# Kernel tuning notes

Hardware: AMD Instinct MI355X
Metric: run time of the kernel (lower is better)

## Reference

```python
import jax, jax.numpy as jnp
import numpy as np

NUM_CLASSES = 80
FOCAL_ALPHA = 0.25
FOCAL_GAMMA = 2.0
HUBER_SIGMA = 3.0
REG_MEAN = 0.0
REG_STD = 0.2
IMG_H = 800.0
IMG_W = 800.0
B, A, M = 4, 100000, 32


def setup_inputs() -> dict:
    key = jax.random.key(0)
    k1, k2, k3, k4, k5, k6, k7 = jax.random.split(key, 7)
    classification = jax.random.uniform(k1, (B, A, NUM_CLASSES), dtype=jnp.float32)
    regression = jax.random.normal(k2, (B, A, 4), dtype=jnp.float32)
    # plausible anchors: centers inside image, sizes 16..256
    cx = jax.random.uniform(k3, (A,), minval=0.0, maxval=IMG_W)
    cy = jax.random.uniform(k4, (A,), minval=0.0, maxval=IMG_H)
    s = jax.random.uniform(k5, (A, 2), minval=16.0, maxval=256.0)
    anchors = jnp.stack([cx - s[:, 0] / 2, cy - s[:, 1] / 2,
                         cx + s[:, 0] / 2, cy + s[:, 1] / 2], axis=1).astype(jnp.float32)
    # annotations: [B, M, 5] = x1,y1,x2,y2,class
    xy = jax.random.uniform(k6, (B, M, 2), minval=0.0, maxval=650.0)
    wh = jax.random.uniform(k7, (B, M, 2), minval=30.0, maxval=150.0)
    cls = jax.random.randint(jax.random.fold_in(key, 9), (B, M, 1), 0, NUM_CLASSES).astype(jnp.float32)
    annotations = jnp.concatenate([xy, xy + wh, cls], axis=-1)
    return {"classification": classification, "regression": regression,
            "anchors": anchors, "annotations": annotations}


def _pairwise_iou(anchors, boxes):
    # anchors [A,4], boxes [M,4] -> [A,M]
    ix1 = jnp.maximum(anchors[:, None, 0], boxes[None, :, 0])
    iy1 = jnp.maximum(anchors[:, None, 1], boxes[None, :, 1])
    ix2 = jnp.minimum(anchors[:, None, 2], boxes[None, :, 2])
    iy2 = jnp.minimum(anchors[:, None, 3], boxes[None, :, 3])
    inter = jnp.clip(ix2 - ix1, 0.0) * jnp.clip(iy2 - iy1, 0.0)
    area_a = (anchors[:, 2] - anchors[:, 0]) * (anchors[:, 3] - anchors[:, 1])
    area_b = (boxes[:, 2] - boxes[:, 0]) * (boxes[:, 3] - boxes[:, 1])
    union = area_a[:, None] + area_b[None, :] - inter
    return inter / jnp.maximum(union, 1e-8)


def _targets(anchors, annotations):
    # per-image anchor assignment, vmapped over batch
    def per_image(ann):
        boxes = ann[:, :4]
        cls = ann[:, 4].astype(jnp.int32)
        ious = _pairwise_iou(anchors, boxes)          # [A,M]
        best = jnp.argmax(ious, axis=1)               # [A]
        best_iou = jnp.max(ious, axis=1)
        pos = best_iou >= 0.5
        ign = (best_iou > 0.4) & (~pos)
        states = jnp.where(pos, 1.0, jnp.where(ign, -1.0, 0.0))
        cx = (anchors[:, 0] + anchors[:, 2]) * 0.5
        cy = (anchors[:, 1] + anchors[:, 3]) * 0.5
        inside = (cx >= 0) & (cx < IMG_W) & (cy >= 0) & (cy < IMG_H)
        states = jnp.where(inside, states, -1.0)
        labels = jax.nn.one_hot(cls[best], NUM_CLASSES, dtype=jnp.float32) * pos[:, None]
        ab = boxes[best]                              # assigned gt boxes [A,4]
        aw = anchors[:, 2] - anchors[:, 0]
        ah = anchors[:, 3] - anchors[:, 1]
        t = jnp.stack([(ab[:, 0] - anchors[:, 0]) / aw,
                       (ab[:, 1] - anchors[:, 1]) / ah,
                       (ab[:, 2] - anchors[:, 2]) / aw,
                       (ab[:, 3] - anchors[:, 3]) / ah], axis=1)
        t = (t - REG_MEAN) / REG_STD
        return labels, t, states
    return jax.vmap(per_image)(annotations)


def reference(classification, regression, anchors, annotations):
    labels, reg_t, states = _targets(anchors, annotations)   # [B,A,K],[B,A,4],[B,A]
    num_pos = jnp.maximum(jnp.sum((states == 1.0).astype(jnp.float32)), 1.0)
    # focal loss over non-ignored anchors
    valid = (states != -1.0)[..., None].astype(jnp.float32)
    p = jnp.clip(classification, 1e-4, 1.0 - 1e-4)
    bce = -(labels * jnp.log(p) + (1.0 - labels) * jnp.log1p(-p))
    alpha_f = jnp.where(labels == 1.0, FOCAL_ALPHA, 1.0 - FOCAL_ALPHA)
    focal_w = alpha_f * jnp.where(labels == 1.0, 1.0 - p, p) ** FOCAL_GAMMA
    cls_loss = jnp.sum(focal_w * bce * valid) / num_pos
    # smooth L1 over positive anchors
    pos_m = (states == 1.0)[..., None].astype(jnp.float32)
    s2 = HUBER_SIGMA ** 2
    d = jnp.abs(regression - reg_t)
    l1 = jnp.where(d < 1.0 / s2, 0.5 * s2 * d * d, d - 0.5 / s2)
    reg_loss = jnp.sum(l1 * pos_m) / num_pos
    return cls_loss + reg_loss
```

## Files before the change

kernel.cpp:

```cpp
#include <hip/hip_runtime.h>

#define BB 4
#define AA 100000
#define MM 32
#define NC 80
#define GX 391
#define NBLK (GX * BB)


__global__ __launch_bounds__(256) void fused_kernel(
    const float* __restrict__ anchors,
    const float* __restrict__ annotations,
    const float* __restrict__ regression,
    const float* __restrict__ cls,
    float* __restrict__ cls_part,
    float* __restrict__ reg_part,
    unsigned* __restrict__ pos_part)
{
    __shared__ float ann[MM * 5];
    __shared__ int scode[256];
    const int b = blockIdx.y;
    const int tid = threadIdx.x;
    if (tid < MM * 5) ann[tid] = annotations[b * MM * 5 + tid];
    __syncthreads();

    const int abase = blockIdx.x * 256;
    const int a = abase + tid;
    float reg_sum = 0.0f;
    int pos_cnt = 0;
    int code = -2;

    if (a < AA) {
        const float4 an = ((const float4*)anchors)[a];
        const float ax1 = an.x, ay1 = an.y, ax2 = an.z, ay2 = an.w;
        const float area_a = __fmul_rn(__fsub_rn(ax2, ax1), __fsub_rn(ay2, ay1));

        float best_iou = -1.0f;
        int best = 0;
        #pragma unroll
        for (int j = 0; j < MM; ++j) {
            const float bx1 = ann[j * 5 + 0];
            const float by1 = ann[j * 5 + 1];
            const float bx2 = ann[j * 5 + 2];
            const float by2 = ann[j * 5 + 3];
            const float ix1 = fmaxf(ax1, bx1);
            const float iy1 = fmaxf(ay1, by1);
            const float ix2 = fminf(ax2, bx2);
            const float iy2 = fminf(ay2, by2);
            const float iw = fmaxf(__fsub_rn(ix2, ix1), 0.0f);
            const float ih = fmaxf(__fsub_rn(iy2, iy1), 0.0f);
            const float inter = __fmul_rn(iw, ih);
            const float area_b = __fmul_rn(__fsub_rn(bx2, bx1), __fsub_rn(by2, by1));
            const float uni = __fsub_rn(__fadd_rn(area_a, area_b), inter);
            const float iou = __fdiv_rn(inter, fmaxf(uni, 1e-8f));
            if (iou > best_iou) { best_iou = iou; best = j; }
        }

        const bool pos = best_iou >= 0.5f;
        const bool ign = (best_iou > 0.4f) && !pos;
        const float cx = (ax1 + ax2) * 0.5f;
        const float cy = (ay1 + ay2) * 0.5f;
        const bool inside = (cx >= 0.0f) && (cx < 800.0f) && (cy >= 0.0f) && (cy < 800.0f);

        const bool valid = inside && !ign;
        if (valid) code = pos ? (int)ann[best * 5 + 4] : -1;

        if (pos && inside) {
            pos_cnt = 1;
            const float aw = ax2 - ax1;
            const float ah = ay2 - ay1;
            const float bx1 = ann[best * 5 + 0];
            const float by1 = ann[best * 5 + 1];
            const float bx2 = ann[best * 5 + 2];
            const float by2 = ann[best * 5 + 3];
            float t[4];
            t[0] = ((bx1 - ax1) / aw) / 0.2f;
            t[1] = ((by1 - ay1) / ah) / 0.2f;
            t[2] = ((bx2 - ax2) / aw) / 0.2f;
            t[3] = ((by2 - ay2) / ah) / 0.2f;
            const float* rg = regression + (((size_t)b * AA + a) * 4);
            #pragma unroll
            for (int k = 0; k < 4; ++k) {
                const float d = fabsf(rg[k] - t[k]);
                reg_sum += (d < (1.0f / 9.0f)) ? (4.5f * d * d) : (d - (0.5f / 9.0f));
            }
        }
    }
    scode[tid] = code;
    __syncthreads();

    float csum = 0.0f;
    const float4* base4 = (const float4*)cls + ((size_t)b * AA + abase) * 20;
    const int maxflat = (abase + 256 <= AA) ? (5120 - 1) : ((AA - abase) * 20 - 1);

    #pragma unroll
    for (int batch = 0; batch < 4; ++batch) {
        float4 v[5];
        #pragma unroll
        for (int k = 0; k < 5; ++k) {
            const int flat = (batch * 5 + k) * 256 + tid;
            v[k] = base4[min(flat, maxflat)];
        }
        #pragma unroll
        for (int k = 0; k < 5; ++k) {
            const int flat = (batch * 5 + k) * 256 + tid;
            const int s = flat / 20;
            const int colb = (flat - s * 20) * 4;
            const int c = scode[s];
            const float m = (c != -2) ? 1.0f : 0.0f;
            const float px[4] = { v[k].x, v[k].y, v[k].z, v[k].w };
            float pc[4];
            float sub = 0.0f;
            #pragma unroll
            for (int j = 0; j < 4; ++j) {
                const float p = fminf(fmaxf(px[j], 1e-4f), 0.9999f);
                pc[j] = p;
                sub += 0.75f * p * p * (-__logf(1.0f - p));
            }
            csum += m * sub;
            const unsigned rel = (unsigned)(c - colb);
            if (rel < 4u) {
                const float p = pc[rel];
                const float onem = 1.0f - p;
                csum += 0.25f * onem * onem * (-__logf(p))
                      - 0.75f * p * p * (-__logf(onem));
            }
        }
    }

    #pragma unroll
    for (int off = 32; off > 0; off >>= 1) {
        csum    += __shfl_down(csum, off);
        reg_sum += __shfl_down(reg_sum, off);
        pos_cnt += __shfl_down(pos_cnt, off);
    }
    __shared__ float wc[4], wr[4];
    __shared__ int   wp[4];
    const int wave = tid >> 6, lane = tid & 63;
    if (lane == 0) { wc[wave] = csum; wr[wave] = reg_sum; wp[wave] = pos_cnt; }
    __syncthreads();
    if (tid == 0) {
        const int idx = b * GX + blockIdx.x;
        cls_part[idx] = wc[0] + wc[1] + wc[2] + wc[3];
        reg_part[idx] = wr[0] + wr[1] + wr[2] + wr[3];
        pos_part[idx] = (unsigned)(wp[0] + wp[1] + wp[2] + wp[3]);
    }
}

__global__ __launch_bounds__(256) void finalize_kernel(
    const float* __restrict__ cls_part,
    const float* __restrict__ reg_part,
    const unsigned* __restrict__ pos_part,
    float* __restrict__ out)
{
    float cs = 0.0f, rs = 0.0f;
    unsigned pc = 0;
    for (int i = threadIdx.x; i < NBLK; i += 256) {
        cs += cls_part[i];
        rs += reg_part[i];
        pc += pos_part[i];
    }
    #pragma unroll
    for (int off = 32; off > 0; off >>= 1) {
        cs += __shfl_down(cs, off);
        rs += __shfl_down(rs, off);
        pc += __shfl_down(pc, off);
    }
    __shared__ float wc[4], wr[4];
    __shared__ unsigned wp[4];
    const int wave = threadIdx.x >> 6, lane = threadIdx.x & 63;
    if (lane == 0) { wc[wave] = cs; wr[wave] = rs; wp[wave] = pc; }
    __syncthreads();
    if (threadIdx.x == 0) {
        const float csum = wc[0] + wc[1] + wc[2] + wc[3];
        const float rsum = wr[0] + wr[1] + wr[2] + wr[3];
        const float np = fmaxf((float)(wp[0] + wp[1] + wp[2] + wp[3]), 1.0f);
        out[0] = (csum + rsum) / np;
    }
}

extern "C" void kernel_launch(void* const* d_in, const int* in_sizes, int n_in,
                              void* d_out, int out_size, void* d_ws, size_t ws_size,
                              hipStream_t stream)
{
    const float* classification = (const float*)d_in[0];
    const float* regression     = (const float*)d_in[1];
    const float* anchors        = (const float*)d_in[2];
    const float* annotations    = (const float*)d_in[3];
    float* out = (float*)d_out;

    float*    cls_part = (float*)d_ws;
    float*    reg_part = cls_part + NBLK;
    unsigned* pos_part = (unsigned*)(reg_part + NBLK);

    dim3 grid(GX, BB);
    fused_kernel<<<grid, 256, 0, stream>>>(anchors, annotations, regression,
                                           classification, cls_part, reg_part, pos_part);
    finalize_kernel<<<1, 256, 0, stream>>>(cls_part, reg_part, pos_part, out);
}
```

Before: 203.2 us.

## Prefetch classification loads before IoU matching and precompute box areas

Issues the first ten float4 loads of the classification tile before the IoU/anchor-assignment phase, with a sched_barrier so they stay in flight while the matching runs. The remaining two batches are software-pipelined, each loaded one batch ahead of the focal computation. Box areas are precomputed once into shared memory, and the focal code is rewritten as macros with a select chain in place of dynamic array indexing. Launch bounds now request 4 blocks per CU. The early loads raise register pressure, which may hurt occupancy or cause spills.

```diff
diff --git a/kernel.cpp b/kernel.cpp
--- a/kernel.cpp
+++ b/kernel.cpp
@@ -8,7 +8,40 @@
 #define NBLK (GX * BB)
 
 
-__global__ __launch_bounds__(256) void fused_kernel(
+#define FOCAL_K(vk, flatk)                                                  \
+  {                                                                         \
+    const int s    = (flatk) / 20;                                          \
+    const int colb = ((flatk) - s * 20) * 4;                                \
+    const int c    = scode[s];                                              \
+    const float m  = (c != -2) ? 1.0f : 0.0f;                               \
+    const float q0 = fminf(fmaxf((vk).x, 1e-4f), 0.9999f);                  \
+    const float q1 = fminf(fmaxf((vk).y, 1e-4f), 0.9999f);                  \
+    const float q2 = fminf(fmaxf((vk).z, 1e-4f), 0.9999f);                  \
+    const float q3 = fminf(fmaxf((vk).w, 1e-4f), 0.9999f);                  \
+    float sub = 0.0f;                                                       \
+    sub += 0.75f * q0 * q0 * (-__logf(1.0f - q0));                          \
+    sub += 0.75f * q1 * q1 * (-__logf(1.0f - q1));                          \
+    sub += 0.75f * q2 * q2 * (-__logf(1.0f - q2));                          \
+    sub += 0.75f * q3 * q3 * (-__logf(1.0f - q3));                          \
+    csum += m * sub;                                                        \
+    const unsigned rel = (unsigned)(c - colb);                              \
+    if (rel < 4u) {      \
+      const float p = (rel & 2u) ? ((rel & 1u) ? q3 : q2)                   \
+                                 : ((rel & 1u) ? q1 : q0);                  \
+      const float onem = 1.0f - p;                                          \
+      csum += 0.25f * onem * onem * (-__logf(p))                            \
+            - 0.75f * p * p * (-__logf(onem));                              \
+    }                                                                       \
+  }
+
+#define FOCAL_BATCH(vv, batch)                                              \
+  _Pragma("unroll")                                                         \
+  for (int k = 0; k < 5; ++k) {                                             \
+    const int flat = ((batch) * 5 + k) * 256 + tid;                         \
+    FOCAL_K((vv)[k], flat)                                                  \
+  }
+
+__global__ __launch_bounds__(256, 4) void fused_kernel(
     const float* __restrict__ anchors,
     const float* __restrict__ annotations,
     const float* __restrict__ regression,
@@ -18,14 +51,33 @@
     unsigned* __restrict__ pos_part)
 {
     __shared__ float ann[MM * 5];
+    __shared__ float areab[MM];
     __shared__ int scode[256];
     const int b = blockIdx.y;
     const int tid = threadIdx.x;
     if (tid < MM * 5) ann[tid] = annotations[b * MM * 5 + tid];
+    if (tid < MM) {
+        const float bx1 = annotations[b * MM * 5 + tid * 5 + 0];
+        const float by1 = annotations[b * MM * 5 + tid * 5 + 1];
+        const float bx2 = annotations[b * MM * 5 + tid * 5 + 2];
+        const float by2 = annotations[b * MM * 5 + tid * 5 + 3];
+        areab[tid] = __fmul_rn(__fsub_rn(bx2, bx1), __fsub_rn(by2, by1));
+    }
     __syncthreads();
 
     const int abase = blockIdx.x * 256;
     const int a = abase + tid;
+
+    const float4* base4 = (const float4*)cls + ((size_t)b * AA + abase) * 20;
+    const int maxflat = (abase + 256 <= AA) ? (5120 - 1) : ((AA - abase) * 20 - 1);
+
+    float4 vA[5], vB[5];
+    #pragma unroll
+    for (int k = 0; k < 5; ++k) vA[k] = base4[min(k * 256 + tid, maxflat)];
+    #pragma unroll
+    for (int k = 0; k < 5; ++k) vB[k] = base4[min((5 + k) * 256 + tid, maxflat)];
+    __builtin_amdgcn_sched_barrier(0);
+
     float reg_sum = 0.0f;
     int pos_cnt = 0;
     int code = -2;
@@ -50,8 +102,7 @@
             const float iw = fmaxf(__fsub_rn(ix2, ix1), 0.0f);
             const float ih = fmaxf(__fsub_rn(iy2, iy1), 0.0f);
             const float inter = __fmul_rn(iw, ih);
-            const float area_b = __fmul_rn(__fsub_rn(bx2, bx1), __fsub_rn(by2, by1));
-            const float uni = __fsub_rn(__fadd_rn(area_a, area_b), inter);
+            const float uni = __fsub_rn(__fadd_rn(area_a, areab[j]), inter);
             const float iou = __fdiv_rn(inter, fmaxf(uni, 1e-8f));
             if (iou > best_iou) { best_iou = iou; best = j; }
         }
@@ -90,43 +141,20 @@
     __syncthreads();
 
     float csum = 0.0f;
-    const float4* base4 = (const float4*)cls + ((size_t)b * AA + abase) * 20;
-    const int maxflat = (abase + 256 <= AA) ? (5120 - 1) : ((AA - abase) * 20 - 1);
-
-    #pragma unroll
-    for (int batch = 0; batch < 4; ++batch) {
-        float4 v[5];
-        #pragma unroll
-        for (int k = 0; k < 5; ++k) {
-            const int flat = (batch * 5 + k) * 256 + tid;
-            v[k] = base4[min(flat, maxflat)];
-        }
-        #pragma unroll
-        for (int k = 0; k < 5; ++k) {
-            const int flat = (batch * 5 + k) * 256 + tid;
-            const int s = flat / 20;
-            const int colb = (flat - s * 20) * 4;
-            const int c = scode[s];
-            const float m = (c != -2) ? 1.0f : 0.0f;
-            const float px[4] = { v[k].x, v[k].y, v[k].z, v[k].w };
-            float pc[4];
-            float sub = 0.0f;
-            #pragma unroll
-            for (int j = 0; j < 4; ++j) {
-                const float p = fminf(fmaxf(px[j], 1e-4f), 0.9999f);
-                pc[j] = p;
-                sub += 0.75f * p * p * (-__logf(1.0f - p));
-            }
-            csum += m * sub;
-            const unsigned rel = (unsigned)(c - colb);
-            if (rel < 4u) {
-                const float p = pc[rel];
-                const float onem = 1.0f - p;
-                csum += 0.25f * onem * onem * (-__logf(p))
-                      - 0.75f * p * p * (-__logf(onem));
-            }
-        }
-    }
+
+    float4 vC[5];
+    #pragma unroll
+    for (int k = 0; k < 5; ++k) vC[k] = base4[min((10 + k) * 256 + tid, maxflat)];
+
+    FOCAL_BATCH(vA, 0)
+
+    float4 vD[5];
+    #pragma unroll
+    for (int k = 0; k < 5; ++k) vD[k] = base4[min((15 + k) * 256 + tid, maxflat)];
+
+    FOCAL_BATCH(vB, 1)
+    FOCAL_BATCH(vC, 2)
+    FOCAL_BATCH(vD, 3)
 
     #pragma unroll
     for (int off = 32; off > 0; off >>= 1) {
```

Measured after the change: 209.7 us. +3.2%, slower.
